# Kernel tuning notes

Measured on AMD Instinct MI355X. Metric: run time of the kernel, lower is better.

The kernel has to match this reference:

```python
import jax, jax.numpy as jnp
import numpy as np

N, K, DIN = 2, 2048, 1024
H, DOUT = 16, 64


def setup_inputs() -> dict:
    key = jax.random.key(0)
    ks = jax.random.split(key, 12)
    c_qk = float(np.sqrt(6.0 / (DIN + DOUT)))  # per-head q/k init scale
    c_v = c_qk  # dim_q == dim_v == DOUT here
    u = lambda k, shape, c: jax.random.uniform(k, shape, jnp.float32, -c, c)
    inp = {
        "query": jax.random.normal(ks[0], (N, K, DIN), jnp.float32),
        "key": jax.random.normal(ks[1], (N, K, DIN), jnp.float32),
        "value": jax.random.normal(ks[2], (N, K, DIN), jnp.float32),
        "mask": jax.random.randint(ks[3], (N, K, K), 0, 2) > 0,  # bool (N,K,K)
        # stacked per-head projection weights: (H, DIN, DOUT), biases (H, DOUT)
        "Wq": u(ks[4], (H, DIN, DOUT), c_qk),
        "bq": u(ks[5], (H, DOUT), c_qk),
        "Wk": u(ks[6], (H, DIN, DOUT), c_qk),
        "bk": u(ks[7], (H, DOUT), c_qk),
        "Wv": u(ks[8], (H, DIN, DOUT), c_v),
        "bv": u(ks[9], (H, DOUT), c_v),
        # output projection: (H*DOUT, DIN)
        "Wp": u(ks[10], (H * DOUT, DIN), c_qk),
        "bp": u(ks[11], (DIN,), c_qk),
    }
    return inp


def reference(query, key, value, mask, Wq, bq, Wk, bk, Wv, bv, Wp, bp):
    # Per-head projections, batched over heads: (N,K,DIN) x (H,DIN,DOUT) -> (N,H,K,DOUT)
    q = jnp.einsum("nkm,hmd->nhkd", query, Wq) + bq[None, :, None, :]
    k = jnp.einsum("nkm,hmd->nhkd", key, Wk) + bk[None, :, None, :]
    v = jnp.einsum("nkm,hmd->nhkd", value, Wv) + bv[None, :, None, :]
    # scaled dot-product scores: (N,H,K,K), scaled by sqrt(per-head dim)
    scores = jnp.einsum("nhkd,nhld->nhkl", q, k) / jnp.sqrt(jnp.asarray(DOUT, q.dtype))
    scores = jnp.where(mask[:, None, :, :], jnp.asarray(-1e9, scores.dtype), scores)
    w = jax.nn.softmax(scores, axis=-1)
    y = jnp.einsum("nhkl,nhld->nhkd", w, v)  # (N,H,K,DOUT)
    # concat heads along feature dim (head order matches torch cat over head list)
    y = jnp.transpose(y, (0, 2, 1, 3)).reshape(N, K, H * DOUT)
    return y @ Wp + bp
```

## Files before the change

### kernel.cpp

```cpp
#include <hip/hip_runtime.h>
#include <hip/hip_bf16.h>
#include <stdint.h>

typedef __attribute__((ext_vector_type(8))) __bf16 bf16x8;
typedef __attribute__((ext_vector_type(2))) __bf16 bf16x2;
typedef __attribute__((ext_vector_type(4))) float floatx4;

#define NB 2
#define SEQ 2048
#define DIN 1024
#define NH 16
#define DH 64
#define DMODEL 1024
#define BQ 128
#define BK 64
#define PAD 72
#define QSCALE 0.18033688011112042f

__device__ __forceinline__ float bf2f(unsigned short u) {
    return __uint_as_float(((unsigned)u) << 16);
}
__device__ __forceinline__ unsigned short f2bf(float f) {
    unsigned u = __float_as_uint(f);
    unsigned r = (u + 0x7FFFu + ((u >> 16) & 1u)) >> 16;
    return (unsigned short)r;
}
__device__ __forceinline__ float ldin(const void* p, size_t idx, int isbf) {
    return isbf ? bf2f(((const unsigned short*)p)[idx]) : ((const float*)p)[idx];
}

__device__ __forceinline__ void gl_lds16(const void* g, void* l) {
    __builtin_amdgcn_global_load_lds(
        reinterpret_cast<__attribute__((address_space(1))) unsigned int*>(
            reinterpret_cast<uintptr_t>(g)),
        reinterpret_cast<__attribute__((address_space(3))) unsigned int*>(
            reinterpret_cast<uintptr_t>(l)),
        16, 0, 0);
}

__device__ __forceinline__ int wave_is_bf16(const void* p) {
    unsigned short u = ((const unsigned short*)p)[2 * (threadIdx.x & 63)];
    int e = (u >> 7) & 0xFF;
    int sane = (u == 0 || (e > 100 && e < 140)) ? 1 : 0;
    return __popcll(__ballot(sane)) >= 32;
}
__device__ __forceinline__ int wave_mask_is_int(const void* p) {
    int v = ((const int*)p)[threadIdx.x & 63];
    int zo = (v == 0 || v == 1) ? 1 : 0;
    return __popcll(__ballot(zo)) >= 48;
}

__global__ __launch_bounds__(256) void prep(
    const void* __restrict__ q, const void* __restrict__ k, const void* __restrict__ v,
    const void* __restrict__ mask,
    const void* __restrict__ wq, const void* __restrict__ wk,
    const void* __restrict__ wv, const void* __restrict__ wp,
    unsigned short* __restrict__ a0, unsigned short* __restrict__ a1,
    unsigned short* __restrict__ a2,
    unsigned short* __restrict__ t0, unsigned short* __restrict__ t1,
    unsigned short* __restrict__ t2, unsigned short* __restrict__ t3,
    unsigned int* __restrict__ mbits)
{
    __shared__ float xls[64][68];
    const int b = blockIdx.x;
    const int tid = threadIdx.x;
    if (b < 12288) {
        int z = b >> 12, blk = b & 4095;
        const void* src = (z == 0) ? q : (z == 1) ? k : v;
        unsigned short* dst = (z == 0) ? a0 : (z == 1) ? a1 : a2;
        int isbf = wave_is_bf16(src);
        size_t i = ((size_t)blk * 256 + tid) * 4;
        if (isbf) {
            *(ushort4*)&dst[i] = *(const ushort4*)((const unsigned short*)src + i);
        } else {
            float4 f = *(const float4*)((const float*)src + i);
            ushort4 o;
            o.x = f2bf(f.x); o.y = f2bf(f.y); o.z = f2bf(f.z); o.w = f2bf(f.w);
            *(ushort4*)&dst[i] = o;
        }
    } else if (b < 13312) {
        int blk = b - 12288;
        int w = blk * 256 + tid;
        int is_int = wave_mask_is_int(mask);
        unsigned bits = 0;
        if (is_int) {
            const int4* p = (const int4*)mask + (size_t)w * 8;
#pragma unroll
            for (int g = 0; g < 8; ++g) {
                int4 vv = p[g];
                bits |= (unsigned)(vv.x != 0) << (g * 4 + 0);
                bits |= (unsigned)(vv.y != 0) << (g * 4 + 1);
                bits |= (unsigned)(vv.z != 0) << (g * 4 + 2);
                bits |= (unsigned)(vv.w != 0) << (g * 4 + 3);
            }
        } else {
            const uint4* p = (const uint4*)mask + (size_t)w * 2;
#pragma unroll
            for (int g = 0; g < 2; ++g) {
                uint4 vv = p[g];
                unsigned ws4[4] = {vv.x, vv.y, vv.z, vv.w};
#pragma unroll
                for (int c = 0; c < 4; ++c)
#pragma unroll
                    for (int bb = 0; bb < 4; ++bb)
                        bits |= (unsigned)(((ws4[c] >> (8 * bb)) & 0xFFu) != 0)
                                << (g * 16 + c * 4 + bb);
            }
        }
        mbits[w] = bits;
    } else {
        int zb = b - 13312;
        int z = zb >> 8, t = zb & 255;
        const void* src = (z == 0) ? wq : (z == 1) ? wk : (z == 2) ? wv : wp;
        unsigned short* dst = (z == 0) ? t0 : (z == 1) ? t1 : (z == 2) ? t2 : t3;
        int isbf = wave_is_bf16(src);
        int r = tid >> 2, cs = (tid & 3) * 16;
        if (z < 3) {
            int h = t >> 4, m0 = (t & 15) * 64;
#pragma unroll
            for (int j = 0; j < 16; ++j)
                xls[r][cs + j] = ldin(src, (size_t)h * 65536 + (size_t)(m0 + r) * 64 + cs + j, isbf);
            __syncthreads();
            int d2 = tid >> 2, ms = (tid & 3) * 16;
            size_t orow = (size_t)(h * 64 + d2) * 1024 + m0 + ms;
#pragma unroll
            for (int g = 0; g < 4; ++g) {
                ushort4 o;
                o.x = f2bf(xls[ms + g * 4 + 0][d2]);
                o.y = f2bf(xls[ms + g * 4 + 1][d2]);
                o.z = f2bf(xls[ms + g * 4 + 2][d2]);
                o.w = f2bf(xls[ms + g * 4 + 3][d2]);
                *(ushort4*)&dst[orow + g * 4] = o;
            }
        } else {
            int m0 = (t >> 4) * 64, c0 = (t & 15) * 64;
#pragma unroll
            for (int j = 0; j < 16; ++j)
                xls[r][cs + j] = ldin(src, (size_t)(m0 + r) * 1024 + c0 + cs + j, isbf);
            __syncthreads();
            int d2 = tid >> 2, ms = (tid & 3) * 16;
            size_t orow = (size_t)(c0 + d2) * 1024 + m0 + ms;
#pragma unroll
            for (int g = 0; g < 4; ++g) {
                ushort4 o;
                o.x = f2bf(xls[ms + g * 4 + 0][d2]);
                o.y = f2bf(xls[ms + g * 4 + 1][d2]);
                o.z = f2bf(xls[ms + g * 4 + 2][d2]);
                o.w = f2bf(xls[ms + g * 4 + 3][d2]);
                *(ushort4*)&dst[orow + g * 4] = o;
            }
        }
    }
}

__global__ __launch_bounds__(256) void expand_mask(
    const unsigned int* __restrict__ mbits, unsigned short* __restrict__ m16)
{
    int gid = blockIdx.x * 256 + threadIdx.x;
    unsigned w = mbits[gid];
    unsigned wrd[16];
#pragma unroll
    for (int i = 0; i < 16; ++i) {
        unsigned lo = ((w >> (2 * i)) & 1u) - 1u;
        unsigned hi = ((w >> (2 * i + 1)) & 1u) - 1u;
        wrd[i] = (lo & 0xFFFFu) | (hi << 16);
    }
    uint4* dst = (uint4*)&m16[(size_t)gid * 32];
#pragma unroll
    for (int g = 0; g < 4; ++g) dst[g] = *(uint4*)&wrd[g * 4];
}

__global__ __launch_bounds__(256) void gemm_mfma(
    const unsigned short* __restrict__ A0, const unsigned short* __restrict__ A1,
    const unsigned short* __restrict__ A2,
    const unsigned short* __restrict__ B0, const unsigned short* __restrict__ B1,
    const unsigned short* __restrict__ B2,
    const void* __restrict__ bias0, const void* __restrict__ bias1,
    const void* __restrict__ bias2,
    void* __restrict__ C0, void* __restrict__ C1, void* __restrict__ C2,
    int mode0)
{
    const int z = blockIdx.z;
    const unsigned short* A  = (z == 0) ? A0 : (z == 1) ? A1 : A2;
    const unsigned short* BT = (z == 0) ? B0 : (z == 1) ? B1 : B2;
    const void* bias = (z == 0) ? bias0 : (z == 1) ? bias1 : bias2;
    void* C = (z == 0) ? C0 : (z == 1) ? C1 : C2;
    const int mode = mode0 + z;
    const int isbf = wave_is_bf16(bias);
    const float scl = (mode == 0) ? QSCALE : 1.0f;

    const int n0  = blockIdx.x * 128;
    const int m0g = blockIdx.y * 128;
    const int tid = threadIdx.x;
    const int wave = tid >> 6, lane = tid & 63;
    const int l16 = lane & 15, quad = lane >> 4;
    const int wm = wave & 1, wn = wave >> 1;

    __shared__ __align__(16) unsigned short smem[17408];
    unsigned short* As = smem;
    unsigned short* Bs = smem + 8192;

    floatx4 acc[4][4];
#pragma unroll
    for (int mt = 0; mt < 4; ++mt)
#pragma unroll
        for (int nt = 0; nt < 4; ++nt) acc[mt][nt] = floatx4{0.f, 0.f, 0.f, 0.f};

    const int lrow8 = lane >> 3;
    const int lseg  = (lane & 7) * 8;

    for (int kk = 0; kk < 1024; kk += 64) {
#pragma unroll
        for (int j = 0; j < 4; ++j) {
            int row0 = wave * 8 + j * 32;
            gl_lds16(&A[(size_t)(m0g + row0 + lrow8) * 1024 + kk + lseg], &As[row0 * 64]);
            gl_lds16(&BT[(size_t)(n0 + row0 + lrow8) * 1024 + kk + lseg], &Bs[row0 * 64]);
        }
        __syncthreads();
#pragma unroll
        for (int ks = 0; ks < 2; ++ks) {
            bf16x8 af[4], bf[4];
#pragma unroll
            for (int mt = 0; mt < 4; ++mt)
                af[mt] = *(const bf16x8*)&As[(wm * 64 + mt * 16 + l16) * 64 + ks * 32 + quad * 8];
#pragma unroll
            for (int nt = 0; nt < 4; ++nt)
                bf[nt] = *(const bf16x8*)&Bs[(wn * 64 + nt * 16 + l16) * 64 + ks * 32 + quad * 8];
#pragma unroll
            for (int mt = 0; mt < 4; ++mt)
#pragma unroll
                for (int nt = 0; nt < 4; ++nt)
                    acc[mt][nt] = __builtin_amdgcn_mfma_f32_16x16x32_bf16(af[mt], bf[nt], acc[mt][nt], 0, 0, 0);
        }
        __syncthreads();
    }

    float bv4[4];
#pragma unroll
    for (int nt = 0; nt < 4; ++nt)
        bv4[nt] = ldin(bias, n0 + wn * 64 + nt * 16 + l16, isbf);

    if (mode <= 1) {
        unsigned short* O = (unsigned short*)C;
#pragma unroll
        for (int mt = 0; mt < 4; ++mt)
#pragma unroll
            for (int reg = 0; reg < 4; ++reg) {
                int row = m0g + wm * 64 + mt * 16 + quad * 4 + reg;
                int nb = row >> 11, kq = row & (SEQ - 1);
#pragma unroll
                for (int nt = 0; nt < 4; ++nt) {
                    int c = n0 + wn * 64 + nt * 16 + l16;
                    int h = c >> 6, d = c & 63;
                    O[(((size_t)nb * NH + h) * SEQ + kq) * DH + d] =
                        f2bf((acc[mt][nt][reg] + bv4[nt]) * scl);
                }
            }
    } else if (mode == 2) {
#pragma unroll
        for (int mt = 0; mt < 4; ++mt)
#pragma unroll
            for (int nt = 0; nt < 4; ++nt)
#pragma unroll
                for (int reg = 0; reg < 4; ++reg) {
                    int m_l = wm * 64 + mt * 16 + quad * 4 + reg;
                    int c_l = wn * 64 + nt * 16 + l16;
                    smem[c_l * 136 + m_l] = f2bf(acc[mt][nt][reg] + bv4[nt]);
                }
        __syncthreads();
        unsigned short* O = (unsigned short*)C;
        int nb = m0g >> 11;
        int kq0 = m0g & (SEQ - 1);
#pragma unroll
        for (int j = 0; j < 8; ++j) {
            int i = tid + j * 256;
            int c_l = i >> 4, m8 = (i & 15) * 8;
            int cg = n0 + c_l, h = cg >> 6, d = cg & 63;
            *(bf16x8*)&O[(((size_t)nb * NH + h) * DH + d) * SEQ + kq0 + m8] =
                *(const bf16x8*)&smem[c_l * 136 + m8];
        }
    } else {
        unsigned short* Ob = (unsigned short*)C;
        float* Of = (float*)C;
#pragma unroll
        for (int mt = 0; mt < 4; ++mt)
#pragma unroll
            for (int reg = 0; reg < 4; ++reg) {
                int row = m0g + wm * 64 + mt * 16 + quad * 4 + reg;
#pragma unroll
                for (int nt = 0; nt < 4; ++nt) {
                    int c = n0 + wn * 64 + nt * 16 + l16;
                    float v = acc[mt][nt][reg] + bv4[nt];
                    if (isbf) Ob[(size_t)row * DMODEL + c] = f2bf(v);
                    else      Of[(size_t)row * DMODEL + c] = v;
                }
            }
    }
}

__global__ __launch_bounds__(512) void attn_mfma(
    const unsigned short* __restrict__ qws, const unsigned short* __restrict__ kws,
    const unsigned short* __restrict__ vtws, const unsigned short* __restrict__ m16,
    unsigned short* __restrict__ yws)
{
    const int qt   = blockIdx.x;
    const int h    = blockIdx.y;
    const int n    = blockIdx.z;
    const int tid  = threadIdx.x;
    const int wave = tid >> 6;
    const int lane = tid & 63;
    const int l16  = lane & 15;
    const int quad = lane >> 4;

    __shared__ __align__(16) unsigned short Ks[2][BK * DH];
    __shared__ __align__(16) unsigned short VTs[2][DH * BK];
    __shared__ __align__(16) unsigned short Ps[8][16 * PAD];

    const size_t base_nh = ((size_t)n * NH + h) * SEQ * DH;
    const size_t base_vt = ((size_t)n * NH + h) * DH * SEQ;
    const int q0 = qt * BQ;
    const int qrow = wave * 16 + l16;

    const unsigned short* mrl = m16 + ((size_t)n * SEQ + q0 + qrow) * SEQ;

    const int srow8  = lane >> 3;
    const int schunk = ((lane & 7) ^ srow8) * 8;
    const int swz = l16 & 7;
    int koff[2], voff[2];
#pragma unroll
    for (int ks = 0; ks < 2; ++ks) {
        koff[ks] = l16 * DH + (((ks * 4 + quad) ^ swz) * 8);
        voff[ks] = l16 * BK + (((ks * 4 + quad) ^ swz) * 8);
    }

    bf16x8 vones;
#pragma unroll
    for (int j = 0; j < 8; ++j) vones[j] = (__bf16)1.0f;

    bf16x8 af[2];
    {
        const unsigned short* qp = qws + base_nh + (size_t)(q0 + qrow) * DH + quad * 8;
        af[0] = *(const bf16x8*)qp;
        af[1] = *(const bf16x8*)(qp + 32);
    }

    {
        int rl = wave * 8;
        gl_lds16(&kws[base_nh + (size_t)(rl + srow8) * DH + schunk], &Ks[0][rl * DH]);
        gl_lds16(&vtws[base_vt + (size_t)(rl + srow8) * SEQ + schunk], &VTs[0][rl * BK]);
    }

    floatx4 O[4];
#pragma unroll
    for (int dt = 0; dt < 4; ++dt) O[dt] = floatx4{0.f, 0.f, 0.f, 0.f};
    floatx4 Lacc = floatx4{0.f, 0.f, 0.f, 0.f};

    __syncthreads();

    for (int it = 0; it < SEQ / BK; ++it) {
        const int cur = it & 1, nxt = cur ^ 1;
        const bool has_next = (it + 1) < (SEQ / BK);
        const int j0 = it * BK;
        const int j0n = j0 + BK;

        if (has_next) {
            int rl = wave * 8;
            gl_lds16(&kws[base_nh + (size_t)(j0n + rl + srow8) * DH + schunk], &Ks[nxt][rl * DH]);
            gl_lds16(&vtws[base_vt + (size_t)(rl + srow8) * SEQ + j0n + schunk], &VTs[nxt][rl * BK]);
        }

        uint2 mm[4];
#pragma unroll
        for (int nt = 0; nt < 4; ++nt)
            mm[nt] = *(const uint2*)&mrl[j0 + nt * 16 + quad * 4];

        bf16x8 bfK[4][2];
#pragma unroll
        for (int nt = 0; nt < 4; ++nt)
#pragma unroll
            for (int ks = 0; ks < 2; ++ks)
                bfK[nt][ks] = *(const bf16x8*)&Ks[cur][nt * 16 * DH + koff[ks]];

        float St[4][4];
#pragma unroll
        for (int nt = 0; nt < 4; ++nt) {
            floatx4 c = {0.f, 0.f, 0.f, 0.f};
            c = __builtin_amdgcn_mfma_f32_16x16x32_bf16(bfK[nt][0], af[0], c, 0, 0, 0);
            c = __builtin_amdgcn_mfma_f32_16x16x32_bf16(bfK[nt][1], af[1], c, 0, 0, 0);
            St[nt][0] = c[0]; St[nt][1] = c[1]; St[nt][2] = c[2]; St[nt][3] = c[3];
        }

#pragma unroll
        for (int nt = 0; nt < 4; ++nt) {
            bf16x2 e01, e23;
            e01[0] = (__bf16)__builtin_amdgcn_exp2f(St[nt][0]);
            e01[1] = (__bf16)__builtin_amdgcn_exp2f(St[nt][1]);
            e23[0] = (__bf16)__builtin_amdgcn_exp2f(St[nt][2]);
            e23[1] = (__bf16)__builtin_amdgcn_exp2f(St[nt][3]);
            uint2 pk;
            pk.x = (*(unsigned*)&e01) & mm[nt].x;
            pk.y = (*(unsigned*)&e23) & mm[nt].y;
            *(uint2*)&Ps[wave][l16 * PAD + nt * 16 + quad * 4] = pk;
        }

        bf16x8 pa[2], vb[4][2];
#pragma unroll
        for (int ks = 0; ks < 2; ++ks)
            pa[ks] = *(const bf16x8*)&Ps[wave][l16 * PAD + ks * 32 + quad * 8];
#pragma unroll
        for (int dt = 0; dt < 4; ++dt)
#pragma unroll
            for (int ks = 0; ks < 2; ++ks)
                vb[dt][ks] = *(const bf16x8*)&VTs[cur][dt * 16 * BK + voff[ks]];

        Lacc = __builtin_amdgcn_mfma_f32_16x16x32_bf16(pa[0], vones, Lacc, 0, 0, 0);
        Lacc = __builtin_amdgcn_mfma_f32_16x16x32_bf16(pa[1], vones, Lacc, 0, 0, 0);
#pragma unroll
        for (int dt = 0; dt < 4; ++dt) {
            O[dt] = __builtin_amdgcn_mfma_f32_16x16x32_bf16(pa[0], vb[dt][0], O[dt], 0, 0, 0);
            O[dt] = __builtin_amdgcn_mfma_f32_16x16x32_bf16(pa[1], vb[dt][1], O[dt], 0, 0, 0);
        }

        __syncthreads();
    }

#pragma unroll
    for (int r = 0; r < 4; ++r) {
        float lr = Lacc[r];
        float inv = (lr > 0.f) ? 1.f / lr : 0.f;
        int row = q0 + wave * 16 + quad * 4 + r;
#pragma unroll
        for (int dt = 0; dt < 4; ++dt) {
            int col = h * DH + dt * 16 + l16;
            yws[((size_t)n * SEQ + row) * DMODEL + col] = f2bf(O[dt][r] * inv);
        }
    }
}

extern "C" void kernel_launch(void* const* d_in, const int* in_sizes, int n_in,
                              void* d_out, int out_size, void* d_ws, size_t ws_size,
                              hipStream_t stream) {
    const void* query = d_in[0];
    const void* key_  = d_in[1];
    const void* value = d_in[2];
    const void* mask  = d_in[3];
    const void* Wq = d_in[4];
    const void* bq = d_in[5];
    const void* Wk = d_in[6];
    const void* bk = d_in[7];
    const void* Wv = d_in[8];
    const void* bv = d_in[9];
    const void* Wp = d_in[10];
    const void* bp = d_in[11];

    const size_t per = (size_t)NB * NH * SEQ * DH;
    unsigned short* us = (unsigned short*)d_ws;
    unsigned short* qws  = us;
    unsigned short* kws  = us + per;
    unsigned short* vtws = us + 2 * per;
    unsigned short* abf0 = us + 3 * per;
    unsigned short* abf1 = us + 4 * per;
    unsigned short* abf2 = us + 5 * per;
    unsigned short* wt0  = us + 6 * per;
    unsigned short* wt1  = wt0 + 1048576;
    unsigned short* wt2  = wt1 + 1048576;
    unsigned short* wt3  = wt2 + 1048576;
    unsigned int* mbits  = (unsigned int*)(wt3 + 1048576);
    unsigned short* yws = abf0;
    unsigned short* mask16 = abf1;

    prep<<<dim3(14336), 256, 0, stream>>>(query, key_, value, mask,
                                          Wq, Wk, Wv, Wp,
                                          abf0, abf1, abf2,
                                          wt0, wt1, wt2, wt3, mbits);
    gemm_mfma<<<dim3(8, 32, 3), 256, 0, stream>>>(abf0, abf1, abf2, wt0, wt1, wt2,
                                                  bq, bk, bv, qws, kws, vtws, 0);
    expand_mask<<<dim3(1024), 256, 0, stream>>>(mbits, mask16);
    attn_mfma<<<dim3(SEQ / BQ, NH, NB), 512, 0, stream>>>(qws, kws, vtws, mask16, yws);
    gemm_mfma<<<dim3(8, 32, 1), 256, 0, stream>>>(yws, yws, yws, wt3, wt3, wt3,
                                                  bp, bp, bp, d_out, d_out, d_out, 3);
}
```

Measured before the change: 312.7 us.

## Process two 16-row query groups per wave in attention, halving block threads

The attention kernel now runs 4 waves of 256 threads, each covering 32 query rows as two 16-row groups, instead of 8 waves covering 16 rows each. Each K and V^T fragment read from LDS is reused across both groups, which halves LDS fragment traffic per query row and gives each wave more independent MFMA work. The cost is more accumulator and fragment registers per thread (launch bounds set to 256 threads with 2 blocks minimum), and fewer waves per block to hide latency.

```diff
diff --git a/kernel.cpp b/kernel.cpp
--- a/kernel.cpp
+++ b/kernel.cpp
@@ -298,7 +298,7 @@
     }
 }
 
-__global__ __launch_bounds__(512) void attn_mfma(
+__global__ __launch_bounds__(256, 2) void attn_mfma(
     const unsigned short* __restrict__ qws, const unsigned short* __restrict__ kws,
     const unsigned short* __restrict__ vtws, const unsigned short* __restrict__ m16,
     unsigned short* __restrict__ yws)
@@ -314,14 +314,27 @@
 
     __shared__ __align__(16) unsigned short Ks[2][BK * DH];
     __shared__ __align__(16) unsigned short VTs[2][DH * BK];
-    __shared__ __align__(16) unsigned short Ps[8][16 * PAD];
+    __shared__ __align__(16) unsigned short Ps[4][32 * PAD];
 
     const size_t base_nh = ((size_t)n * NH + h) * SEQ * DH;
     const size_t base_vt = ((size_t)n * NH + h) * DH * SEQ;
     const int q0 = qt * BQ;
-    const int qrow = wave * 16 + l16;
-
-    const unsigned short* mrl = m16 + ((size_t)n * SEQ + q0 + qrow) * SEQ;
+
+    const unsigned short* mrl0;
+    const unsigned short* mrl1;
+    bf16x8 af[2][2];
+    {
+        int qr0 = q0 + wave * 32 + l16;
+        int qr1 = qr0 + 16;
+        mrl0 = m16 + ((size_t)n * SEQ + qr0) * SEQ;
+        mrl1 = m16 + ((size_t)n * SEQ + qr1) * SEQ;
+        const unsigned short* qp0 = qws + base_nh + (size_t)qr0 * DH + quad * 8;
+        const unsigned short* qp1 = qws + base_nh + (size_t)qr1 * DH + quad * 8;
+        af[0][0] = *(const bf16x8*)qp0;
+        af[0][1] = *(const bf16x8*)(qp0 + 32);
+        af[1][0] = *(const bf16x8*)qp1;
+        af[1][1] = *(const bf16x8*)(qp1 + 32);
+    }
 
     const int srow8  = lane >> 3;
     const int schunk = ((lane & 7) ^ srow8) * 8;
@@ -337,23 +350,21 @@
 #pragma unroll
     for (int j = 0; j < 8; ++j) vones[j] = (__bf16)1.0f;
 
-    bf16x8 af[2];
-    {
-        const unsigned short* qp = qws + base_nh + (size_t)(q0 + qrow) * DH + quad * 8;
-        af[0] = *(const bf16x8*)qp;
-        af[1] = *(const bf16x8*)(qp + 32);
-    }
-
-    {
-        int rl = wave * 8;
+#pragma unroll
+    for (int j = 0; j < 2; ++j) {
+        int rl = wave * 16 + j * 8;
         gl_lds16(&kws[base_nh + (size_t)(rl + srow8) * DH + schunk], &Ks[0][rl * DH]);
         gl_lds16(&vtws[base_vt + (size_t)(rl + srow8) * SEQ + schunk], &VTs[0][rl * BK]);
     }
 
-    floatx4 O[4];
-#pragma unroll
-    for (int dt = 0; dt < 4; ++dt) O[dt] = floatx4{0.f, 0.f, 0.f, 0.f};
-    floatx4 Lacc = floatx4{0.f, 0.f, 0.f, 0.f};
+    floatx4 O[2][4];
+#pragma unroll
+    for (int g = 0; g < 2; ++g)
+#pragma unroll
+        for (int dt = 0; dt < 4; ++dt) O[g][dt] = floatx4{0.f, 0.f, 0.f, 0.f};
+    floatx4 Lacc[2];
+    Lacc[0] = floatx4{0.f, 0.f, 0.f, 0.f};
+    Lacc[1] = floatx4{0.f, 0.f, 0.f, 0.f};
 
     __syncthreads();
 
@@ -364,15 +375,20 @@
         const int j0n = j0 + BK;
 
         if (has_next) {
-            int rl = wave * 8;
-            gl_lds16(&kws[base_nh + (size_t)(j0n + rl + srow8) * DH + schunk], &Ks[nxt][rl * DH]);
-            gl_lds16(&vtws[base_vt + (size_t)(rl + srow8) * SEQ + j0n + schunk], &VTs[nxt][rl * BK]);
-        }
-
-        uint2 mm[4];
-#pragma unroll
-        for (int nt = 0; nt < 4; ++nt)
-            mm[nt] = *(const uint2*)&mrl[j0 + nt * 16 + quad * 4];
+#pragma unroll
+            for (int j = 0; j < 2; ++j) {
+                int rl = wave * 16 + j * 8;
+                gl_lds16(&kws[base_nh + (size_t)(j0n + rl + srow8) * DH + schunk], &Ks[nxt][rl * DH]);
+                gl_lds16(&vtws[base_vt + (size_t)(rl + srow8) * SEQ + j0n + schunk], &VTs[nxt][rl * BK]);
+            }
+        }
+
+        uint2 mm[2][4];
+#pragma unroll
+        for (int nt = 0; nt < 4; ++nt) {
+            mm[0][nt] = *(const uint2*)&mrl0[j0 + nt * 16 + quad * 4];
+            mm[1][nt] = *(const uint2*)&mrl1[j0 + nt * 16 + quad * 4];
+        }
 
         bf16x8 bfK[4][2];
 #pragma unroll
@@ -381,60 +397,75 @@
             for (int ks = 0; ks < 2; ++ks)
                 bfK[nt][ks] = *(const bf16x8*)&Ks[cur][nt * 16 * DH + koff[ks]];
 
-        float St[4][4];
+        float St[2][4][4];
 #pragma unroll
         for (int nt = 0; nt < 4; ++nt) {
-            floatx4 c = {0.f, 0.f, 0.f, 0.f};
-            c = __builtin_amdgcn_mfma_f32_16x16x32_bf16(bfK[nt][0], af[0], c, 0, 0, 0);
-            c = __builtin_amdgcn_mfma_f32_16x16x32_bf16(bfK[nt][1], af[1], c, 0, 0, 0);
-            St[nt][0] = c[0]; St[nt][1] = c[1]; St[nt][2] = c[2]; St[nt][3] = c[3];
-        }
-
-#pragma unroll
-        for (int nt = 0; nt < 4; ++nt) {
-            bf16x2 e01, e23;
-            e01[0] = (__bf16)__builtin_amdgcn_exp2f(St[nt][0]);
-            e01[1] = (__bf16)__builtin_amdgcn_exp2f(St[nt][1]);
-            e23[0] = (__bf16)__builtin_amdgcn_exp2f(St[nt][2]);
-            e23[1] = (__bf16)__builtin_amdgcn_exp2f(St[nt][3]);
-            uint2 pk;
-            pk.x = (*(unsigned*)&e01) & mm[nt].x;
-            pk.y = (*(unsigned*)&e23) & mm[nt].y;
-            *(uint2*)&Ps[wave][l16 * PAD + nt * 16 + quad * 4] = pk;
-        }
-
-        bf16x8 pa[2], vb[4][2];
-#pragma unroll
-        for (int ks = 0; ks < 2; ++ks)
-            pa[ks] = *(const bf16x8*)&Ps[wave][l16 * PAD + ks * 32 + quad * 8];
+#pragma unroll
+            for (int g = 0; g < 2; ++g) {
+                floatx4 c = {0.f, 0.f, 0.f, 0.f};
+                c = __builtin_amdgcn_mfma_f32_16x16x32_bf16(bfK[nt][0], af[g][0], c, 0, 0, 0);
+                c = __builtin_amdgcn_mfma_f32_16x16x32_bf16(bfK[nt][1], af[g][1], c, 0, 0, 0);
+                St[g][nt][0] = c[0]; St[g][nt][1] = c[1];
+                St[g][nt][2] = c[2]; St[g][nt][3] = c[3];
+            }
+        }
+
+#pragma unroll
+        for (int g = 0; g < 2; ++g)
+#pragma unroll
+            for (int nt = 0; nt < 4; ++nt) {
+                bf16x2 e01, e23;
+                e01[0] = (__bf16)__builtin_amdgcn_exp2f(St[g][nt][0]);
+                e01[1] = (__bf16)__builtin_amdgcn_exp2f(St[g][nt][1]);
+                e23[0] = (__bf16)__builtin_amdgcn_exp2f(St[g][nt][2]);
+                e23[1] = (__bf16)__builtin_amdgcn_exp2f(St[g][nt][3]);
+                uint2 pk;
+                pk.x = (*(unsigned*)&e01) & mm[g][nt].x;
+                pk.y = (*(unsigned*)&e23) & mm[g][nt].y;
+                *(uint2*)&Ps[wave][(g * 16 + l16) * PAD + nt * 16 + quad * 4] = pk;
+            }
+
+        bf16x8 pa[2][2], vb[4][2];
+#pragma unroll
+        for (int g = 0; g < 2; ++g)
+#pragma unroll
+            for (int ks = 0; ks < 2; ++ks)
+                pa[g][ks] = *(const bf16x8*)&Ps[wave][(g * 16 + l16) * PAD + ks * 32 + quad * 8];
 #pragma unroll
         for (int dt = 0; dt < 4; ++dt)
 #pragma unroll
             for (int ks = 0; ks < 2; ++ks)
                 vb[dt][ks] = *(const bf16x8*)&VTs[cur][dt * 16 * BK + voff[ks]];
 
-        Lacc = __builtin_amdgcn_mfma_f32_16x16x32_bf16(pa[0], vones, Lacc, 0, 0, 0);
-        Lacc = __builtin_amdgcn_mfma_f32_16x16x32_bf16(pa[1], vones, Lacc, 0, 0, 0);
+        Lacc[0] = __builtin_amdgcn_mfma_f32_16x16x32_bf16(pa[0][0], vones, Lacc[0], 0, 0, 0);
+        Lacc[1] = __builtin_amdgcn_mfma_f32_16x16x32_bf16(pa[1][0], vones, Lacc[1], 0, 0, 0);
+        Lacc[0] = __builtin_amdgcn_mfma_f32_16x16x32_bf16(pa[0][1], vones, Lacc[0], 0, 0, 0);
+        Lacc[1] = __builtin_amdgcn_mfma_f32_16x16x32_bf16(pa[1][1], vones, Lacc[1], 0, 0, 0);
 #pragma unroll
         for (int dt = 0; dt < 4; ++dt) {
-            O[dt] = __builtin_amdgcn_mfma_f32_16x16x32_bf16(pa[0], vb[dt][0], O[dt], 0, 0, 0);
-            O[dt] = __builtin_amdgcn_mfma_f32_16x16x32_bf16(pa[1], vb[dt][1], O[dt], 0, 0, 0);
+#pragma unroll
+            for (int g = 0; g < 2; ++g) {
+                O[g][dt] = __builtin_amdgcn_mfma_f32_16x16x32_bf16(pa[g][0], vb[dt][0], O[g][dt], 0, 0, 0);
+                O[g][dt] = __builtin_amdgcn_mfma_f32_16x16x32_bf16(pa[g][1], vb[dt][1], O[g][dt], 0, 0, 0);
+            }
         }
 
         __syncthreads();
     }
 
 #pragma unroll
-    for (int r = 0; r < 4; ++r) {
-        float lr = Lacc[r];
-        float inv = (lr > 0.f) ? 1.f / lr : 0.f;
-        int row = q0 + wave * 16 + quad * 4 + r;
-#pragma unroll
-        for (int dt = 0; dt < 4; ++dt) {
-            int col = h * DH + dt * 16 + l16;
-            yws[((size_t)n * SEQ + row) * DMODEL + col] = f2bf(O[dt][r] * inv);
-        }
-    }
+    for (int g = 0; g < 2; ++g)
+#pragma unroll
+        for (int r = 0; r < 4; ++r) {
+            float lr = Lacc[g][r];
+            float inv = (lr > 0.f) ? 1.f / lr : 0.f;
+            int row = q0 + wave * 32 + g * 16 + quad * 4 + r;
+#pragma unroll
+            for (int dt = 0; dt < 4; ++dt) {
+                int col = h * DH + dt * 16 + l16;
+                yws[((size_t)n * SEQ + row) * DMODEL + col] = f2bf(O[g][dt][r] * inv);
+            }
+        }
 }
 
 extern "C" void kernel_launch(void* const* d_in, const int* in_sizes, int n_in,
@@ -476,7 +507,7 @@
     gemm_mfma<<<dim3(8, 32, 3), 256, 0, stream>>>(abf0, abf1, abf2, wt0, wt1, wt2,
                                                   bq, bk, bv, qws, kws, vtws, 0);
     expand_mask<<<dim3(1024), 256, 0, stream>>>(mbits, mask16);
-    attn_mfma<<<dim3(SEQ / BQ, NH, NB), 512, 0, stream>>>(qws, kws, vtws, mask16, yws);
+    attn_mfma<<<dim3(SEQ / BQ, NH, NB), 256, 0, stream>>>(qws, kws, vtws, mask16, yws);
     gemm_mfma<<<dim3(8, 32, 1), 256, 0, stream>>>(yws, yws, yws, wt3, wt3, wt3,
                                                   bp, bp, bp, d_out, d_out, d_out, 3);
 }
```

After: 310.8 us. No clear change (-0.6%).
